# Kernel optimization log

Hardware: AMD Instinct MI355X
Metric: run time of the kernel (lower is better)

The kernel has to match this reference:

```python
import jax, jax.numpy as jnp
import numpy as np

# ---- fixed config (Linear_mvm defaults, XBAR 64x64) ----
ROW = 64; COL = 64
BIT_SLICE = 2; BIT_STREAM = 1
W_BITS = 16; W_FRAC = 12          # weight_bit_frac = weight_bits//4*3
I_BITS = 16; I_FRAC = 12          # input_bit_frac  = input_bits//4*3
ADC_BIT = 8                       # log2(ROW) + bit_slice (bit_stream==1)
ACM_BITS = 16; ACM_FRAC = 12
BSN = W_BITS // BIT_SLICE         # 8 slices per weight, MSB-first columns
STN = I_BITS // BIT_STREAM        # 16 input bit-streams, LSB-first
IN_F = 1024; OUT_F = 1024; BATCH = 256


def _bit_slice_weight(w_nonneg):
    # w_nonneg: [out, in] nonnegative -> sliced crossbar matrix [in, out*BSN] (MSB->LSB per channel)
    w_int = jnp.clip(jnp.round(w_nonneg * (2.0 ** W_FRAC)), 0.0, 2.0 ** W_BITS - 1.0)
    shifts = (BIT_SLICE * (BSN - 1 - jnp.arange(BSN))).astype(jnp.float32)
    sl = jnp.floor(w_int[..., None] / (2.0 ** shifts)) % (2 ** BIT_SLICE)  # [out,in,BSN]
    o, i = w_nonneg.shape
    return sl.transpose(1, 0, 2).reshape(i, o * BSN)


def _input_bits(x):
    # two's-complement fixed point, LSB-first bit planes: [b, in, STN]
    x_int = jnp.clip(jnp.round(x * (2.0 ** I_FRAC)), -(2.0 ** (I_BITS - 1)), 2.0 ** (I_BITS - 1) - 1.0)
    x_u = jnp.where(x_int < 0, x_int + 2.0 ** I_BITS, x_int)
    return jnp.floor(x_u[..., None] / (2.0 ** jnp.arange(I_BITS, dtype=jnp.float32))) % 2.0


def _tile(mat, r, c):
    # pad to tile multiples and reshape to [xr, xc, r, c]
    pr = (-mat.shape[0]) % r; pc = (-mat.shape[1]) % c
    m = jnp.pad(mat, ((0, pr), (0, pc)))
    xr, xc = m.shape[0] // r, m.shape[1] // c
    return m.reshape(xr, r, xc, c).transpose(0, 2, 1, 3)


def _adc(a):
    # uniform ADC quantization of the analog column current to ADC_BIT bits
    full = float(ROW * (2 ** BIT_SLICE - 1))
    step = full / (2.0 ** ADC_BIT - 1.0)
    return jnp.clip(jnp.round(a / step) * step, 0.0, full)


def _mvm_one_sign(bits_tiled, xbars):
    # bits_tiled [b, xr, ROW, STN]; xbars [xr, xc, ROW, COL]
    sw_slice = 2.0 ** (BIT_SLICE * (BSN - 1 - jnp.arange(BSN, dtype=jnp.float32)))  # MSB..LSB
    sw_stream = 2.0 ** (BIT_STREAM * jnp.arange(STN, dtype=jnp.float32))
    sw_stream = sw_stream.at[-1].multiply(-1.0)  # two's-complement MSB stream

    def step(acc, si):
        bi, w = si                                   # bi [b,xr,ROW]
        analog = jnp.einsum('brk,rckj->brcj', bi, xbars)  # [b,xr,xc,COL]
        analog = _adc(analog)
        b, xr, xc, _ = analog.shape
        dig = analog.reshape(b, xr, xc, COL // BSN, BSN) @ sw_slice  # shift-add slices
        return acc + w * dig, None

    b = bits_tiled.shape[0]; xr, xc = xbars.shape[0], xbars.shape[1]
    acc0 = jnp.zeros((b, xr, xc, COL // BSN), jnp.float32)
    streams = jnp.moveaxis(bits_tiled, -1, 0)  # [STN, b, xr, ROW]
    acc, _ = jax.lax.scan(step, acc0, (streams, sw_stream))
    return acc.sum(axis=1).reshape(b, xc * (COL // BSN))  # sum row tiles, flatten channels


def _forward(x, weight, bias):
    pos = _bit_slice_weight(jnp.maximum(weight, 0.0))
    neg = _bit_slice_weight(-jnp.minimum(weight, 0.0))
    xb_pos = _tile(pos, ROW, COL)
    xb_neg = _tile(neg, ROW, COL)
    bits = _input_bits(x)                                  # [b,in,STN]
    xr = xb_pos.shape[0]
    bits = jnp.pad(bits, ((0, 0), (0, xr * ROW - bits.shape[1]), (0, 0)))
    bits = bits.reshape(x.shape[0], xr, ROW, STN)
    out = _mvm_one_sign(bits, xb_pos) - _mvm_one_sign(bits, xb_neg)
    out = out * (2.0 ** (-(W_FRAC + I_FRAC)))              # undo fixed-point scaling
    # accumulator quantization to ACM_BITS / ACM_FRAC
    out = jnp.clip(jnp.round(out * 2.0 ** ACM_FRAC), -(2.0 ** (ACM_BITS - 1)), 2.0 ** (ACM_BITS - 1) - 1.0) * 2.0 ** (-ACM_FRAC)
    out = out[:, :OUT_F]
    return out + bias[None, :]


def setup_inputs() -> dict:
    key = jax.random.key(0)
    k1, k2, k3 = jax.random.split(key, 3)
    x = jax.random.normal(k1, (BATCH, IN_F), jnp.float32)
    weight = jax.random.normal(k2, (OUT_F, IN_F), jnp.float32) * 0.05  # representable in Q4.12
    bias = jax.random.normal(k3, (OUT_F,), jnp.float32) * 0.05
    return {"x": x, "weight": weight, "bias": bias}


def reference(x, weight, bias):
    return _forward(x, weight, bias)
```

## Files before the change

### kernel.cpp

```cpp
#include <hip/hip_runtime.h>
#include <stdint.h>

#define BATCH 256
#define IN_F  1024
#define OUT_F 1024
#define RT    16
#define STN   16
#define NCOL  16384

typedef int   v4i  __attribute__((ext_vector_type(4)));
typedef int   v16i __attribute__((ext_vector_type(16)));
typedef float v2f  __attribute__((ext_vector_type(2)));

#define AP_SZ ((size_t)STN * BATCH * IN_F)
#define BP_SZ ((size_t)64 * NCOL * 16)

__global__ __launch_bounds__(256) void pack_fused(
    const float* __restrict__ x, const float* __restrict__ w,
    uint8_t* __restrict__ Ap2, uint8_t* __restrict__ Bp,
    uint32_t* __restrict__ flags)
{
    if (blockIdx.x < 512) {
        int item = blockIdx.x * 256 + threadIdx.x;
        int o  = item & 1023;
        int sg = (item >> 10) & 1;
        int g  = item >> 11;
        int l  = threadIdx.x & 63;
        const float* wr = w + (size_t)o * IN_F + g * 16;
        uint32_t wq[16];
        #pragma unroll
        for (int j = 0; j < 16; ++j) {
            float wv = wr[j];
            float wf = rintf(fmaxf(sg ? -wv : wv, 0.0f) * 4096.0f);
            wq[j] = (uint32_t)fminf(wf, 65535.0f);
        }
        uint32_t nzmask = 0;
        #pragma unroll
        for (int s = 0; s < 8; ++s) {
            int sh = 14 - 2 * s;
            uint32_t dw[4], nz = 0;
            #pragma unroll
            for (int q = 0; q < 4; ++q) {
                uint32_t d = 0;
                #pragma unroll
                for (int j = 0; j < 4; ++j)
                    d |= ((wq[q * 4 + j] >> sh) & 3u) << (8 * j);
                dw[q] = d;
                nz |= d;
            }
            int sgs = sg * 8 + s;
            *(uint4*)(Bp + (size_t)(g * NCOL + sgs * 1024 + o) * 16) =
                make_uint4(dw[0], dw[1], dw[2], dw[3]);
            nzmask |= (nz ? 1u : 0u) << s;
        }
        int r = g >> 2;
        #pragma unroll
        for (int s = 0; s < 8; ++s) {
            unsigned long long bal = __ballot((int)((nzmask >> s) & 1u));
            uint32_t lo = (uint32_t)bal, hi = (uint32_t)(bal >> 32);
            int sgs = sg * 8 + s;
            if (l == 0 && lo)  atomicOr(&flags[sgs * 32 + (o >> 5)], 1u << r);
            if (l == 32 && hi) atomicOr(&flags[sgs * 32 + (o >> 5)], 1u << r);
        }
    } else {
        int item = (blockIdx.x - 512) * 256 + threadIdx.x;
        int b  = item & 255;
        int tq = (item >> 8) & 3;
        int kg = item >> 10;
        int r = kg >> 2, f = (kg >> 1) & 1, hi = kg & 1;
        int y = b >> 5, l = hi * 32 + (b & 31);
        const float* xr = x + (size_t)b * IN_F + kg * 16;
        uint32_t xu[16];
        #pragma unroll
        for (int j = 0; j < 16; ++j) {
            float xf = rintf(xr[j] * 4096.0f);
            xf = fminf(fmaxf(xf, -32768.0f), 32767.0f);
            xu[j] = (uint32_t)((int)xf) & 0xFFFFu;
        }
        uint8_t* wbase = Ap2 + ((size_t)(r * 8 + y) * 16) * 2048 + f * 1024 + l * 16;
        #pragma unroll
        for (int tt = 0; tt < 4; ++tt) {
            int t = tq * 4 + tt;
            uint32_t dw[4];
            #pragma unroll
            for (int q = 0; q < 4; ++q) {
                uint32_t d = 0;
                #pragma unroll
                for (int j = 0; j < 4; ++j)
                    d |= ((xu[q * 4 + j] >> t) & 1u) << (8 * j);
                dw[q] = d;
            }
            *(uint4*)(wbase + t * 2048) = make_uint4(dw[0], dw[1], dw[2], dw[3]);
        }
    }
}

__global__ __launch_bounds__(512) void cim_block(
    const uint8_t* __restrict__ Ap2, const uint8_t* __restrict__ Bp,
    const uint32_t* __restrict__ flags, const float* __restrict__ bias,
    float* __restrict__ out)
{
    __shared__ __align__(16) uint8_t Abuf[2][32768];
    const float MAG = 12582912.0f;
    int tid = threadIdx.x, wid = tid >> 6, l = tid & 63, h2 = l >> 5;
    int oq = blockIdx.x, y = blockIdx.y;

    uint32_t fw = flags[(l & 15) * 32 + oq];
    uint32_t rmask = fw;
    #pragma unroll
    for (int st = 1; st < 16; st <<= 1)
        rmask |= __shfl_xor(rmask, st, 64);

    v2f acc2[8];
    #pragma unroll
    for (int i = 0; i < 8; ++i) acc2[i] = (v2f)0.0f;
    v16i zero;
    #pragma unroll
    for (int i = 0; i < 16; ++i) zero[i] = 0;

    #define STAGE(BUF, R)                                                     \
        do {                                                                  \
            const uint8_t* sbase = Ap2 + (size_t)((R) * 8 + y) * 32768;       \
            _Pragma("unroll")                                                 \
            for (int ii = 0; ii < 4; ++ii) {                                  \
                int chunk = wid * 4 + ii;                                     \
                __builtin_amdgcn_global_load_lds(                             \
                    (const __attribute__((address_space(1))) uint32_t*)       \
                        (sbase + chunk * 1024 + l * 16),                      \
                    (__attribute__((address_space(3))) uint32_t*)             \
                        (&Abuf[BUF][0] + chunk * 1024),                       \
                    16, 0, 0);                                                \
            }                                                                 \
        } while (0)

    int cnt = 0, cur = 0;
    uint32_t rm = rmask;
    if (rm) STAGE(0, __builtin_ctz(rm));
    __syncthreads();

    while (rm) {
        int r = __builtin_ctz(rm);
        rm &= rm - 1;
        if (rm) STAGE(cur ^ 1, __builtin_ctz(rm));

        uint32_t smask = (uint32_t)__ballot((int)((fw >> r) & 1u)) & 0xFFFFu;
        while (smask) {
            int sgs = __builtin_ctz(smask);
            smask &= smask - 1;
            if ((cnt++ & 7) != wid) continue;

            int s = sgs & 7, sg = sgs >> 3;
            float clane = __int_as_float((141 - 2 * s) << 23) * (192.0f / 255.0f);
            if (sg) clane = -clane;
            int col = sgs * 1024 + oq * 32 + (l & 31);

            v4i bf0 = *(const v4i*)(Bp + ((size_t)(r * 4 + h2)     * NCOL + col) * 16);
            v4i bf1 = *(const v4i*)(Bp + ((size_t)(r * 4 + 2 + h2) * NCOL + col) * 16);

            const uint8_t* abase = &Abuf[cur][0] + l * 16;
            #pragma unroll 4
            for (int t = 0; t < STN; ++t) {
                v4i af0 = *(const v4i*)(abase + t * 2048);
                v4i af1 = *(const v4i*)(abase + t * 2048 + 1024);
                v16i c = __builtin_amdgcn_mfma_i32_32x32x32_i8(af0, bf0, zero, 0, 0, 0);
                c      = __builtin_amdgcn_mfma_i32_32x32x32_i8(af1, bf1, c,    0, 0, 0);
                float wt = (t == 15) ? -32768.0f : (float)(1 << t);
                float cw = clane * wt;
                #pragma unroll
                for (int i = 0; i < 8; ++i) {
                    v2f af; af.x = (float)c[2 * i]; af.y = (float)c[2 * i + 1];
                    v2f tq;
                    tq.x = fmaf(af.x, 1.328125f, MAG);
                    tq.y = fmaf(af.y, 1.328125f, MAG);
                    v2f qf = tq - MAG;
                    acc2[i].x = fmaf(qf.x, cw, acc2[i].x);
                    acc2[i].y = fmaf(qf.y, cw, acc2[i].y);
                }
            }
            __asm__ volatile("" ::: "memory");
        }
        __syncthreads();
        cur ^= 1;
    }

    float* red = (float*)&Abuf[0][0];
    __syncthreads();
    #pragma unroll
    for (int i = 0; i < 16; ++i) {
        float v = (i & 1) ? acc2[i >> 1].y : acc2[i >> 1].x;
        red[wid * 1024 + i * 64 + l] = v;
    }
    __syncthreads();
    #pragma unroll
    for (int k = 0; k < 2; ++k) {
        int i = wid * 2 + k;
        float v = 0.0f;
        #pragma unroll
        for (int w8 = 0; w8 < 8; ++w8) v += red[w8 * 1024 + i * 64 + l];
        int b = y * 32 + (i & 3) + 8 * (i >> 2) + 4 * h2;
        int o = oq * 32 + (l & 31);
        float ov = v * 0x1p-24f;
        float q = rintf(ov * 4096.0f);
        q = fminf(fmaxf(q, -32768.0f), 32767.0f);
        out[(size_t)b * OUT_F + o] = q * 0x1p-12f + bias[o];
    }
}

extern "C" void kernel_launch(void* const* d_in, const int* in_sizes, int n_in,
                              void* d_out, int out_size, void* d_ws, size_t ws_size,
                              hipStream_t stream) {
    const float* x    = (const float*)d_in[0];
    const float* w    = (const float*)d_in[1];
    const float* bias = (const float*)d_in[2];
    float* out = (float*)d_out;

    uint8_t*  Ap2   = (uint8_t*)d_ws;
    uint8_t*  Bp    = Ap2 + AP_SZ;
    uint32_t* flags = (uint32_t*)(Bp + BP_SZ);

    hipMemsetAsync(flags, 0, 512 * sizeof(uint32_t), stream);
    hipLaunchKernelGGL(pack_fused, dim3(768), dim3(256), 0, stream,
                       x, w, Ap2, Bp, flags);
    hipLaunchKernelGGL(cim_block, dim3(32, 8), dim3(512), 0, stream,
                       Ap2, Bp, flags, bias, out);
}
```

Measured before the change: 191.6 us.

## Drop LDS staging of input bit-planes, double waves per block, remap pack indexing

The compute kernel no longer stages input bit-planes into shared memory with double-buffered global_load_lds and barriers. Each wave now reads A fragments straight from global memory (L2), and the block grows to 16 waves so the slice/sign work is spread over more waves, with a 16-way shared-memory reduction at the end. The pack kernel remaps thread indexing so consecutive threads cover consecutive k-groups, which coalesces the weight and x reads. Each wave now computes the row-group mask with a single ballot and one atomicOr instead of per-lane atomics. The risks are higher global/L2 traffic for A, since it is re-read per wave, and register pressure at 1024 threads per block.

```diff
diff --git a/kernel.cpp b/kernel.cpp
--- a/kernel.cpp
+++ b/kernel.cpp
@@ -22,10 +22,9 @@
 {
     if (blockIdx.x < 512) {
         int item = blockIdx.x * 256 + threadIdx.x;
-        int o  = item & 1023;
-        int sg = (item >> 10) & 1;
-        int g  = item >> 11;
-        int l  = threadIdx.x & 63;
+        int g  = item & 63;
+        int o  = (item >> 6) & 1023;
+        int sg = item >> 16;
         const float* wr = w + (size_t)o * IN_F + g * 16;
         uint32_t wq[16];
         #pragma unroll
@@ -34,7 +33,6 @@
             float wf = rintf(fmaxf(sg ? -wv : wv, 0.0f) * 4096.0f);
             wq[j] = (uint32_t)fminf(wf, 65535.0f);
         }
-        uint32_t nzmask = 0;
         #pragma unroll
         for (int s = 0; s < 8; ++s) {
             int sh = 14 - 2 * s;
@@ -51,24 +49,25 @@
             int sgs = sg * 8 + s;
             *(uint4*)(Bp + (size_t)(g * NCOL + sgs * 1024 + o) * 16) =
                 make_uint4(dw[0], dw[1], dw[2], dw[3]);
-            nzmask |= (nz ? 1u : 0u) << s;
-        }
-        int r = g >> 2;
-        #pragma unroll
-        for (int s = 0; s < 8; ++s) {
-            unsigned long long bal = __ballot((int)((nzmask >> s) & 1u));
-            uint32_t lo = (uint32_t)bal, hi = (uint32_t)(bal >> 32);
-            int sgs = sg * 8 + s;
-            if (l == 0 && lo)  atomicOr(&flags[sgs * 32 + (o >> 5)], 1u << r);
-            if (l == 32 && hi) atomicOr(&flags[sgs * 32 + (o >> 5)], 1u << r);
+            unsigned long long bal = __ballot((int)(nz != 0));
+            if ((threadIdx.x & 63) == 0 && bal) {
+                unsigned long long t = bal | (bal >> 1);
+                t |= t >> 2;
+                t &= 0x1111111111111111ULL;
+                uint32_t r16 = 0;
+                #pragma unroll
+                for (int i = 0; i < 16; ++i)
+                    r16 |= (uint32_t)((t >> (4 * i)) & 1ULL) << i;
+                atomicOr(&flags[sgs * 32 + (o >> 5)], r16);
+            }
         }
     } else {
         int item = (blockIdx.x - 512) * 256 + threadIdx.x;
-        int b  = item & 255;
-        int tq = (item >> 8) & 3;
-        int kg = item >> 10;
+        int kg = item & 63;
+        int tq = (item >> 6) & 3;
+        int b  = item >> 8;
         int r = kg >> 2, f = (kg >> 1) & 1, hi = kg & 1;
-        int y = b >> 5, l = hi * 32 + (b & 31);
+        int y = b >> 5, l16 = hi * 32 + (b & 31);
         const float* xr = x + (size_t)b * IN_F + kg * 16;
         uint32_t xu[16];
         #pragma unroll
@@ -77,7 +76,7 @@
             xf = fminf(fmaxf(xf, -32768.0f), 32767.0f);
             xu[j] = (uint32_t)((int)xf) & 0xFFFFu;
         }
-        uint8_t* wbase = Ap2 + ((size_t)(r * 8 + y) * 16) * 2048 + f * 1024 + l * 16;
+        uint8_t* wbase = Ap2 + ((size_t)(r * 8 + y) * 16) * 2048 + f * 1024 + l16 * 16;
         #pragma unroll
         for (int tt = 0; tt < 4; ++tt) {
             int t = tq * 4 + tt;
@@ -95,12 +94,12 @@
     }
 }
 
-__global__ __launch_bounds__(512) void cim_block(
+__global__ __launch_bounds__(1024, 4) void cim_block(
     const uint8_t* __restrict__ Ap2, const uint8_t* __restrict__ Bp,
     const uint32_t* __restrict__ flags, const float* __restrict__ bias,
     float* __restrict__ out)
 {
-    __shared__ __align__(16) uint8_t Abuf[2][32768];
+    __shared__ float red[16 * 1024];
     const float MAG = 12582912.0f;
     int tid = threadIdx.x, wid = tid >> 6, l = tid & 63, h2 = l >> 5;
     int oq = blockIdx.x, y = blockIdx.y;
@@ -118,36 +117,16 @@
     #pragma unroll
     for (int i = 0; i < 16; ++i) zero[i] = 0;
 
-    #define STAGE(BUF, R)                                                     \
-        do {                                                                  \
-            const uint8_t* sbase = Ap2 + (size_t)((R) * 8 + y) * 32768;       \
-            _Pragma("unroll")                                                 \
-            for (int ii = 0; ii < 4; ++ii) {                                  \
-                int chunk = wid * 4 + ii;                                     \
-                __builtin_amdgcn_global_load_lds(                             \
-                    (const __attribute__((address_space(1))) uint32_t*)       \
-                        (sbase + chunk * 1024 + l * 16),                      \
-                    (__attribute__((address_space(3))) uint32_t*)             \
-                        (&Abuf[BUF][0] + chunk * 1024),                       \
-                    16, 0, 0);                                                \
-            }                                                                 \
-        } while (0)
-
-    int cnt = 0, cur = 0;
+    int cnt = 0;
     uint32_t rm = rmask;
-    if (rm) STAGE(0, __builtin_ctz(rm));
-    __syncthreads();
-
     while (rm) {
         int r = __builtin_ctz(rm);
         rm &= rm - 1;
-        if (rm) STAGE(cur ^ 1, __builtin_ctz(rm));
-
         uint32_t smask = (uint32_t)__ballot((int)((fw >> r) & 1u)) & 0xFFFFu;
         while (smask) {
             int sgs = __builtin_ctz(smask);
             smask &= smask - 1;
-            if ((cnt++ & 7) != wid) continue;
+            if ((cnt++ & 15) != wid) continue;
 
             int s = sgs & 7, sg = sgs >> 3;
             float clane = __int_as_float((141 - 2 * s) << 23) * (192.0f / 255.0f);
@@ -157,7 +136,7 @@
             v4i bf0 = *(const v4i*)(Bp + ((size_t)(r * 4 + h2)     * NCOL + col) * 16);
             v4i bf1 = *(const v4i*)(Bp + ((size_t)(r * 4 + 2 + h2) * NCOL + col) * 16);
 
-            const uint8_t* abase = &Abuf[cur][0] + l * 16;
+            const uint8_t* abase = Ap2 + (size_t)(r * 8 + y) * 32768 + l * 16;
             #pragma unroll 4
             for (int t = 0; t < STN; ++t) {
                 v4i af0 = *(const v4i*)(abase + t * 2048);
@@ -177,26 +156,20 @@
                     acc2[i].y = fmaf(qf.y, cw, acc2[i].y);
                 }
             }
-            __asm__ volatile("" ::: "memory");
         }
-        __syncthreads();
-        cur ^= 1;
     }
 
-    float* red = (float*)&Abuf[0][0];
-    __syncthreads();
     #pragma unroll
     for (int i = 0; i < 16; ++i) {
         float v = (i & 1) ? acc2[i >> 1].y : acc2[i >> 1].x;
         red[wid * 1024 + i * 64 + l] = v;
     }
     __syncthreads();
-    #pragma unroll
-    for (int k = 0; k < 2; ++k) {
-        int i = wid * 2 + k;
+    {
+        int i = wid;
         float v = 0.0f;
         #pragma unroll
-        for (int w8 = 0; w8 < 8; ++w8) v += red[w8 * 1024 + i * 64 + l];
+        for (int w16 = 0; w16 < 16; ++w16) v += red[w16 * 1024 + i * 64 + l];
         int b = y * 32 + (i & 3) + 8 * (i >> 2) + 4 * h2;
         int o = oq * 32 + (l & 31);
         float ov = v * 0x1p-24f;
@@ -221,6 +194,6 @@
     hipMemsetAsync(flags, 0, 512 * sizeof(uint32_t), stream);
     hipLaunchKernelGGL(pack_fused, dim3(768), dim3(256), 0, stream,
                        x, w, Ap2, Bp, flags);
-    hipLaunchKernelGGL(cim_block, dim3(32, 8), dim3(512), 0, stream,
+    hipLaunchKernelGGL(cim_block, dim3(32, 8), dim3(1024), 0, stream,
                        Ap2, Bp, flags, bias, out);
 }
```

New measurement: 165.5 us. -13.6%, faster.
